# Optimization experiments

Hardware: AMD Instinct MI355X
Metric: run time of the kernel (lower is better)

The kernel has to match this reference:

```python
import jax, jax.numpy as jnp
import numpy as np

HEAD_NUM = 16
HIDDEN = 1024
HEAD_DIM = HIDDEN // HEAD_NUM


def setup_inputs() -> dict:
    key = jax.random.key(0)
    ks = jax.random.split(key, 9)
    B, S, D = 1, 4096, HIDDEN
    scale = 1.0 / np.sqrt(D)
    inp = {
        "x": jax.random.normal(ks[0], (B, S, D), jnp.float32),
        "wq": jax.random.normal(ks[1], (D, D), jnp.float32) * scale,
        "bq": jnp.zeros((D,), jnp.float32),
        "wk": jax.random.normal(ks[2], (D, D), jnp.float32) * scale,
        "bk": jnp.zeros((D,), jnp.float32),
        "wv": jax.random.normal(ks[3], (D, D), jnp.float32) * scale,
        "bv": jnp.zeros((D,), jnp.float32),
        "wo": jax.random.normal(ks[4], (D, D), jnp.float32) * scale,
        "bo": jnp.zeros((D,), jnp.float32),
    }
    return inp


def reference(x, wq, bq, wk, bk, wv, bv, wo, bo):
    B, S, D = x.shape
    H, Hd = HEAD_NUM, HEAD_DIM
    # QKV projections (weights stored as [in, out])
    q = (x @ wq + bq).reshape(B, S, H, Hd).transpose(0, 2, 1, 3)  # [B,H,S,Hd]
    k = (x @ wk + bk).reshape(B, S, H, Hd).transpose(0, 2, 1, 3)
    v = (x @ wv + bv).reshape(B, S, H, Hd).transpose(0, 2, 1, 3)
    scores = jnp.einsum("bhqd,bhkd->bhqk", q, k) / jnp.sqrt(jnp.float32(Hd))
    attn = jax.nn.softmax(scores, axis=-1)  # dropout in eval mode = identity
    out = jnp.einsum("bhqk,bhkd->bhqd", attn, v)
    out = out.transpose(0, 2, 1, 3).reshape(B, S, D)
    return out @ wo + bo
```

## Files before the change

### kernel.cpp

```cpp
#include <hip/hip_runtime.h>

#define S_LEN  4096
#define DMODEL 1024
#define NHEAD  16
#define HDIM   64

#define QSCALE 0.18033688011112042f

typedef unsigned short u16;
typedef unsigned int   u32;
typedef __bf16 bf16x8 __attribute__((ext_vector_type(8)));
typedef float  f32x4  __attribute__((ext_vector_type(4)));

static __device__ __forceinline__ u16 f2b(float f) {
    union { __bf16 b; u16 u; } c; c.b = (__bf16)f; return c.u;
}

static __device__ __forceinline__ float fexp2(float x) {
#if __has_builtin(__builtin_amdgcn_exp2f)
    return __builtin_amdgcn_exp2f(x);
#else
    return __expf(x * 0.6931471805599453f);
#endif
}

typedef __attribute__((address_space(3))) u32 lds_u32_t;
typedef __attribute__((address_space(1))) const u32 glb_u32_t;
static __device__ __forceinline__ void gload_lds16(const u16* g, u16* l) {
    __builtin_amdgcn_global_load_lds((glb_u32_t*)g, (lds_u32_t*)l, 16, 0, 0);
}

__global__ __launch_bounds__(256)
void convert_x(const float* __restrict__ x, u16* __restrict__ xb) {
    const int i0 = (blockIdx.x * 256 + threadIdx.x) * 8;
    float4 a = *reinterpret_cast<const float4*>(x + i0);
    float4 b = *reinterpret_cast<const float4*>(x + i0 + 4);
    u16 o[8] = {f2b(a.x), f2b(a.y), f2b(a.z), f2b(a.w),
                f2b(b.x), f2b(b.y), f2b(b.z), f2b(b.w)};
    *reinterpret_cast<uint4*>(xb + i0) = *reinterpret_cast<uint4*>(o);
}

__global__ __launch_bounds__(256)
void transpose_w4(const float* __restrict__ w0, const float* __restrict__ w1,
                  const float* __restrict__ w2, const float* __restrict__ w3,
                  u16* __restrict__ wT) {
    const int z = blockIdx.z;
    const float* w = (z == 0) ? w0 : (z == 1) ? w1 : (z == 2) ? w2 : w3;
    u16* dst0 = wT + (size_t)z * DMODEL * DMODEL;
    const int k0 = blockIdx.x * 64, n0 = blockIdx.y * 64;
    const int t = threadIdx.x;
    __shared__ u16 T[64][72];
    const int kk = t >> 4, nn = (t & 15) * 4;
    #pragma unroll
    for (int i = 0; i < 4; ++i) {
        float4 v = *reinterpret_cast<const float4*>(w + (size_t)(k0 + kk + i * 16) * DMODEL + n0 + nn);
        T[nn + 0][kk + i * 16] = f2b(v.x);
        T[nn + 1][kk + i * 16] = f2b(v.y);
        T[nn + 2][kk + i * 16] = f2b(v.z);
        T[nn + 3][kk + i * 16] = f2b(v.w);
    }
    __syncthreads();
    const int n = t >> 2, kc = (t & 3) * 16;
    uint4 r0 = *reinterpret_cast<const uint4*>(&T[n][kc]);
    uint4 r1 = *reinterpret_cast<const uint4*>(&T[n][kc + 8]);
    u16* dst = dst0 + (size_t)(n0 + n) * DMODEL + k0 + kc;
    *reinterpret_cast<uint4*>(dst)     = r0;
    *reinterpret_cast<uint4*>(dst + 8) = r1;
}

__global__ __launch_bounds__(256, 2)
void gemm_qkv(const u16* __restrict__ A, const u16* __restrict__ BT,
              const float* __restrict__ b0, const float* __restrict__ b1,
              const float* __restrict__ b2, u16* __restrict__ Cout) {
    const int m0 = blockIdx.x * 128;
    const int ny = blockIdx.y;
    const int tz = ny >> 3;
    const int n0 = (ny & 7) * 128;
    const int tid = threadIdx.x, lane = tid & 63, w = tid >> 6;
    const int wr = w >> 1, wc = w & 1;
    const int fm = lane & 15, fq = lane >> 4;

    __shared__ u16 As[128][32];
    __shared__ u16 Bs[128][32];

    const u16* Bb = BT + (size_t)tz * DMODEL * DMODEL;

    f32x4 acc[4][4];
    #pragma unroll
    for (int i = 0; i < 4; ++i)
        #pragma unroll
        for (int t = 0; t < 4; ++t) acc[i][t] = f32x4{0.f, 0.f, 0.f, 0.f};

    const int srow = lane >> 2, scol = (lane & 3) * 8;

    for (int k0 = 0; k0 < DMODEL; k0 += 32) {
        #pragma unroll
        for (int r = 0; r < 2; ++r) {
            const int rowA = w * 32 + r * 16;
            gload_lds16(A  + (size_t)(m0 + rowA + srow) * DMODEL + k0 + scol, &As[rowA][0]);
            gload_lds16(Bb + (size_t)(n0 + rowA + srow) * DMODEL + k0 + scol, &Bs[rowA][0]);
        }
        __syncthreads();
        bf16x8 af[4], bf[4];
        #pragma unroll
        for (int i = 0; i < 4; ++i) af[i] = *reinterpret_cast<const bf16x8*>(&As[wr * 64 + i * 16 + fm][fq * 8]);
        #pragma unroll
        for (int t = 0; t < 4; ++t) bf[t] = *reinterpret_cast<const bf16x8*>(&Bs[wc * 64 + t * 16 + fm][fq * 8]);
        #pragma unroll
        for (int i = 0; i < 4; ++i)
            #pragma unroll
            for (int t = 0; t < 4; ++t)
                acc[i][t] = __builtin_amdgcn_mfma_f32_16x16x32_bf16(af[i], bf[t], acc[i][t], 0, 0, 0);
        __syncthreads();
    }

    const float* bp = (tz == 0) ? b0 : (tz == 1) ? b1 : b2;
    u16* base = Cout + (size_t)tz * S_LEN * DMODEL;
    const float scl = (tz == 0) ? QSCALE : 1.0f;
    #pragma unroll
    for (int t = 0; t < 4; ++t) {
        const int col = n0 + wc * 64 + t * 16 + fm;
        const int hh = col >> 6, d = col & 63;
        const float bias = bp[col];
        if (tz == 2) {
            u16* vb = base + ((size_t)hh * HDIM + d) * S_LEN;
            #pragma unroll
            for (int i = 0; i < 4; ++i) {
                const int row0 = m0 + wr * 64 + i * 16 + fq * 4;
                u16 o[4] = {f2b(acc[i][t][0] + bias), f2b(acc[i][t][1] + bias),
                            f2b(acc[i][t][2] + bias), f2b(acc[i][t][3] + bias)};
                *reinterpret_cast<uint2*>(vb + row0) = *reinterpret_cast<uint2*>(o);
            }
        } else {
            #pragma unroll
            for (int i = 0; i < 4; ++i) {
                #pragma unroll
                for (int r = 0; r < 4; ++r) {
                    const int row = m0 + wr * 64 + i * 16 + fq * 4 + r;
                    base[((size_t)hh * S_LEN + row) * HDIM + d] =
                        f2b((acc[i][t][r] + bias) * scl);
                }
            }
        }
    }
}

__global__ __launch_bounds__(256, 2)
void gemm_o(const u16* __restrict__ A, const u16* __restrict__ BT,
            const float* __restrict__ bias, float* __restrict__ C) {
    const int m0 = blockIdx.x * 128;
    const int n0 = blockIdx.y * 64;
    const int tid = threadIdx.x, lane = tid & 63, w = tid >> 6;
    const int fm = lane & 15, fq = lane >> 4;

    __shared__ u16 As[128][32];
    __shared__ u16 Bs[64][32];

    f32x4 acc[2][4];
    #pragma unroll
    for (int i = 0; i < 2; ++i)
        #pragma unroll
        for (int t = 0; t < 4; ++t) acc[i][t] = f32x4{0.f, 0.f, 0.f, 0.f};

    const int srow = lane >> 2, scol = (lane & 3) * 8;

    for (int k0 = 0; k0 < DMODEL; k0 += 32) {
        #pragma unroll
        for (int r = 0; r < 2; ++r) {
            const int rowA = w * 32 + r * 16;
            gload_lds16(A + (size_t)(m0 + rowA + srow) * DMODEL + k0 + scol, &As[rowA][0]);
        }
        gload_lds16(BT + (size_t)(n0 + w * 16 + srow) * DMODEL + k0 + scol, &Bs[w * 16][0]);
        __syncthreads();
        bf16x8 af[2], bf[4];
        #pragma unroll
        for (int i = 0; i < 2; ++i) af[i] = *reinterpret_cast<const bf16x8*>(&As[w * 32 + i * 16 + fm][fq * 8]);
        #pragma unroll
        for (int t = 0; t < 4; ++t) bf[t] = *reinterpret_cast<const bf16x8*>(&Bs[t * 16 + fm][fq * 8]);
        #pragma unroll
        for (int i = 0; i < 2; ++i)
            #pragma unroll
            for (int t = 0; t < 4; ++t)
                acc[i][t] = __builtin_amdgcn_mfma_f32_16x16x32_bf16(af[i], bf[t], acc[i][t], 0, 0, 0);
        __syncthreads();
    }

    #pragma unroll
    for (int t = 0; t < 4; ++t) {
        const int col = n0 + t * 16 + fm;
        const float b = bias[col];
        #pragma unroll
        for (int i = 0; i < 2; ++i) {
            #pragma unroll
            for (int r = 0; r < 4; ++r) {
                const int row = m0 + w * 32 + i * 16 + fq * 4 + r;
                C[(size_t)row * DMODEL + col] = acc[i][t][r] + b;
            }
        }
    }
}

template<int NSPLIT>
__global__ __launch_bounds__(256, 4)
void attn_kernel(const u16* __restrict__ Q, const u16* __restrict__ K,
                 const u16* __restrict__ V, void* __restrict__ Optr,
                 float* __restrict__ Lp) {
    int qt, h, sp;
    if (NSPLIT > 1) {
        const int bid = blockIdx.x;
        const int xcd = bid & 7;
        const int g = bid >> 3;
        qt = g & 31;
        const int hs = g >> 5;
        h = xcd | ((hs & 1) << 3);
        sp = hs >> 1;
    } else {
        qt = blockIdx.x; h = blockIdx.y; sp = 0;
    }
    const int tid = threadIdx.x, lane = tid & 63, wid = tid >> 6;
    const int fm = lane & 15, fq = lane >> 4;

    __shared__ alignas(16) u16 Pt[128][36];
    __shared__ alignas(16) u16 Ks[64][68];
    __shared__ alignas(16) u16 Vt[64][68];

    const u16* Qh = Q + (size_t)h * S_LEN * HDIM;
    const u16* Kh = K + (size_t)h * S_LEN * HDIM;
    const u16* Vh = V + (size_t)h * S_LEN * HDIM;

    const int srow = tid >> 2, sch = (tid & 3) * 16;

    bf16x8 qf[2][2];
    #pragma unroll
    for (int rb = 0; rb < 2; ++rb) {
        const u16* qsrc = Qh + (size_t)(qt * 128 + wid * 32 + rb * 16 + fm) * HDIM + fq * 8;
        qf[rb][0] = *reinterpret_cast<const bf16x8*>(qsrc);
        qf[rb][1] = *reinterpret_cast<const bf16x8*>(qsrc + 32);
    }

    float rsum[2] = {0.f, 0.f};
    f32x4 oacc[2][4];
    #pragma unroll
    for (int rb = 0; rb < 2; ++rb)
        #pragma unroll
        for (int t = 0; t < 4; ++t) oacc[rb][t] = f32x4{0.f, 0.f, 0.f, 0.f};

    const int TOT  = S_LEN / 64;
    const int NT   = TOT / NSPLIT;
    const int kt0  = sp * NT;

    uint4 kr0, kr1, vr0, vr1;
    {
        const u16* ks = Kh + (size_t)(kt0 * 64 + srow) * HDIM + sch;
        kr0 = *reinterpret_cast<const uint4*>(ks);
        kr1 = *reinterpret_cast<const uint4*>(ks + 8);
        const u16* vs = Vh + (size_t)srow * S_LEN + kt0 * 64 + sch;
        vr0 = *reinterpret_cast<const uint4*>(vs);
        vr1 = *reinterpret_cast<const uint4*>(vs + 8);
    }

    for (int it = 0; it < NT; ++it) {
        const int kt = kt0 + it;
        __syncthreads();
        *reinterpret_cast<uint4*>(&Ks[srow][sch])     = kr0;
        *reinterpret_cast<uint4*>(&Ks[srow][sch + 8]) = kr1;
        *reinterpret_cast<uint4*>(&Vt[srow][sch])     = vr0;
        *reinterpret_cast<uint4*>(&Vt[srow][sch + 8]) = vr1;
        __syncthreads();

        if (it + 1 < NT) {
            const u16* ks = Kh + (size_t)((kt + 1) * 64 + srow) * HDIM + sch;
            kr0 = *reinterpret_cast<const uint4*>(ks);
            kr1 = *reinterpret_cast<const uint4*>(ks + 8);
            const u16* vs = Vh + (size_t)srow * S_LEN + (kt + 1) * 64 + sch;
            vr0 = *reinterpret_cast<const uint4*>(vs);
            vr1 = *reinterpret_cast<const uint4*>(vs + 8);
        }

        f32x4 sacc[2][4];
        #pragma unroll
        for (int rb = 0; rb < 2; ++rb)
            #pragma unroll
            for (int mt = 0; mt < 4; ++mt) sacc[rb][mt] = f32x4{0.f, 0.f, 0.f, 0.f};
        __builtin_amdgcn_s_setprio(1);
        #pragma unroll
        for (int kk2 = 0; kk2 < 2; ++kk2) {
            #pragma unroll
            for (int mt = 0; mt < 4; ++mt) {
                bf16x8 kf = *reinterpret_cast<const bf16x8*>(&Ks[mt * 16 + fm][kk2 * 32 + fq * 8]);
                #pragma unroll
                for (int rb = 0; rb < 2; ++rb)
                    sacc[rb][mt] = __builtin_amdgcn_mfma_f32_16x16x32_bf16(kf, qf[rb][kk2], sacc[rb][mt], 0, 0, 0);
            }
        }
        __builtin_amdgcn_s_setprio(0);

        #pragma unroll
        for (int ph = 0; ph < 2; ++ph) {
            #pragma unroll
            for (int rb = 0; rb < 2; ++rb) {
                #pragma unroll
                for (int m2 = 0; m2 < 2; ++m2) {
                    const int mt = ph * 2 + m2;
                    u32 pk[2];
                    float e0 = fexp2(sacc[rb][mt][0]);
                    float e1 = fexp2(sacc[rb][mt][1]);
                    float e2 = fexp2(sacc[rb][mt][2]);
                    float e3 = fexp2(sacc[rb][mt][3]);
                    rsum[rb] += (e0 + e1) + (e2 + e3);
                    pk[0] = (u32)f2b(e0) | ((u32)f2b(e1) << 16);
                    pk[1] = (u32)f2b(e2) | ((u32)f2b(e3) << 16);
                    *reinterpret_cast<uint2*>(&Pt[wid * 32 + rb * 16 + fm][m2 * 16 + fq * 4]) =
                        uint2{pk[0], pk[1]};
                }
            }
            bf16x8 af[2];
            #pragma unroll
            for (int rb = 0; rb < 2; ++rb)
                af[rb] = *reinterpret_cast<const bf16x8*>(&Pt[wid * 32 + rb * 16 + fm][fq * 8]);
            __builtin_amdgcn_s_setprio(1);
            #pragma unroll
            for (int t = 0; t < 4; ++t) {
                bf16x8 bf = *reinterpret_cast<const bf16x8*>(&Vt[t * 16 + fm][ph * 32 + fq * 8]);
                #pragma unroll
                for (int rb = 0; rb < 2; ++rb)
                    oacc[rb][t] = __builtin_amdgcn_mfma_f32_16x16x32_bf16(af[rb], bf, oacc[rb][t], 0, 0, 0);
            }
            __builtin_amdgcn_s_setprio(0);
        }
    }

    if (NSPLIT > 1) {
        float* Op = (float*)Optr + (size_t)sp * S_LEN * DMODEL;
        #pragma unroll
        for (int rb = 0; rb < 2; ++rb) {
            float rs = rsum[rb];
            rs += __shfl_xor(rs, 16, 64);
            rs += __shfl_xor(rs, 32, 64);
            if (fq == 0)
                Lp[(size_t)sp * NHEAD * S_LEN + (size_t)h * S_LEN +
                   qt * 128 + wid * 32 + rb * 16 + fm] = rs;
            #pragma unroll
            for (int t = 0; t < 4; ++t) {
                const int d = t * 16 + fm;
                #pragma unroll
                for (int r = 0; r < 4; ++r) {
                    const int row = qt * 128 + wid * 32 + rb * 16 + fq * 4 + r;
                    Op[(size_t)row * DMODEL + h * HDIM + d] = oacc[rb][t][r];
                }
            }
        }
    } else {
        float l[2][4];
        #pragma unroll
        for (int rb = 0; rb < 2; ++rb) {
            float rs = rsum[rb];
            rs += __shfl_xor(rs, 16, 64);
            rs += __shfl_xor(rs, 32, 64);
            #pragma unroll
            for (int r = 0; r < 4; ++r) l[rb][r] = __shfl(rs, fq * 4 + r, 64);
        }
        u16* O = (u16*)Optr;
        #pragma unroll
        for (int rb = 0; rb < 2; ++rb)
            #pragma unroll
            for (int t = 0; t < 4; ++t) {
                const int d = t * 16 + fm;
                #pragma unroll
                for (int r = 0; r < 4; ++r) {
                    const int row = qt * 128 + wid * 32 + rb * 16 + fq * 4 + r;
                    O[(size_t)row * DMODEL + h * HDIM + d] = f2b(oacc[rb][t][r] / l[rb][r]);
                }
            }
    }
}

template<int NS>
__global__ __launch_bounds__(256)
void combine_o(const float* __restrict__ Op, const float* __restrict__ Lp,
               u16* __restrict__ Ob) {
    const size_t i = ((size_t)blockIdx.x * 256 + threadIdx.x) * 4;
    const int row = (int)(i >> 10), col = (int)(i & 1023);
    const int h = col >> 6;
    float ax = 0.f, ay = 0.f, az = 0.f, aw = 0.f, l = 0.f;
    #pragma unroll
    for (int s = 0; s < NS; ++s) {
        float4 v = *reinterpret_cast<const float4*>(Op + (size_t)s * S_LEN * DMODEL + i);
        ax += v.x; ay += v.y; az += v.z; aw += v.w;
        l += Lp[(size_t)s * NHEAD * S_LEN + (size_t)h * S_LEN + row];
    }
    const float inv = 1.0f / l;
    u16 o[4] = {f2b(ax * inv), f2b(ay * inv), f2b(az * inv), f2b(aw * inv)};
    *reinterpret_cast<uint2*>(Ob + i) = *reinterpret_cast<uint2*>(o);
}

extern "C" void kernel_launch(void* const* d_in, const int* in_sizes, int n_in,
                              void* d_out, int out_size, void* d_ws, size_t ws_size,
                              hipStream_t stream) {
    const float* x  = (const float*)d_in[0];
    const float* wq = (const float*)d_in[1];
    const float* bq = (const float*)d_in[2];
    const float* wk = (const float*)d_in[3];
    const float* bk = (const float*)d_in[4];
    const float* wv = (const float*)d_in[5];
    const float* bv = (const float*)d_in[6];
    const float* wo = (const float*)d_in[7];
    const float* bo = (const float*)d_in[8];

    u16* ws = (u16*)d_ws;
    const size_t MW  = (size_t)DMODEL * DMODEL;
    const size_t NX  = (size_t)S_LEN * DMODEL;
    const size_t TSZ = (size_t)NHEAD * S_LEN * HDIM;

    u16* xb = ws;
    u16* WT = xb + NX;
    u16* Qb = WT + 4 * MW;
    u16* Ob = Qb + 3 * TSZ;
    float* Op = (float*)(Ob + NX);
    float* Lp2 = Op + (size_t)2 * NX;
    const size_t need2 = (size_t)((char*)(Lp2 + (size_t)2 * NHEAD * S_LEN) - (char*)d_ws);

    hipLaunchKernelGGL(convert_x, dim3(NX / 2048), dim3(256), 0, stream, x, xb);
    hipLaunchKernelGGL(transpose_w4, dim3(16, 16, 4), dim3(256), 0, stream, wq, wk, wv, wo, WT);

    hipLaunchKernelGGL(gemm_qkv, dim3(S_LEN / 128, 24), dim3(256), 0, stream,
                       xb, WT, bq, bk, bv, Qb);

    if (ws_size >= need2) {
        hipLaunchKernelGGL((attn_kernel<2>), dim3(1024), dim3(256), 0, stream,
                           Qb, Qb + TSZ, Qb + 2 * TSZ, (void*)Op, Lp2);
        hipLaunchKernelGGL((combine_o<2>), dim3((S_LEN * DMODEL / 4) / 256), dim3(256), 0, stream,
                           Op, Lp2, Ob);
    } else {
        hipLaunchKernelGGL((attn_kernel<1>), dim3(S_LEN / 128, NHEAD), dim3(256), 0, stream,
                           Qb, Qb + TSZ, Qb + 2 * TSZ, (void*)Ob, (float*)nullptr);
    }

    hipLaunchKernelGGL(gemm_o, dim3(S_LEN / 128, DMODEL / 64), dim3(256), 0, stream,
                       Ob, WT + 3 * MW, bo, (float*)d_out);
}
```

Measured before the change: 244.1 us.

## Load V fragments directly from global memory and double-buffer K tiles in LDS

Removes the V tile staging through shared memory. Each wave now loads its MFMA B-operand fragments for V straight from global (transposed V layout) into registers, issuing the second half after the QK MFMAs. K is double-buffered in LDS, which drops one of the two barriers per iteration. The cost is that every wave redundantly fetches the same V data from global/L2 instead of sharing one LDS copy, and register pressure rises.

Measured after the change: 347.7 us. +42.4%, slower.

```diff
diff --git a/kernel.cpp b/kernel.cpp
--- a/kernel.cpp
+++ b/kernel.cpp
@@ -221,8 +221,7 @@
     const int fm = lane & 15, fq = lane >> 4;
 
     __shared__ alignas(16) u16 Pt[128][36];
-    __shared__ alignas(16) u16 Ks[64][68];
-    __shared__ alignas(16) u16 Vt[64][68];
+    __shared__ alignas(16) u16 Ks[2][64][68];
 
     const u16* Qh = Q + (size_t)h * S_LEN * HDIM;
     const u16* Kh = K + (size_t)h * S_LEN * HDIM;
@@ -249,32 +248,34 @@
     const int NT   = TOT / NSPLIT;
     const int kt0  = sp * NT;
 
-    uint4 kr0, kr1, vr0, vr1;
+    const u16* vbase = Vh + (size_t)fm * S_LEN + (size_t)kt0 * 64 + fq * 8;
+
+    uint4 kr0, kr1;
     {
         const u16* ks = Kh + (size_t)(kt0 * 64 + srow) * HDIM + sch;
         kr0 = *reinterpret_cast<const uint4*>(ks);
         kr1 = *reinterpret_cast<const uint4*>(ks + 8);
-        const u16* vs = Vh + (size_t)srow * S_LEN + kt0 * 64 + sch;
-        vr0 = *reinterpret_cast<const uint4*>(vs);
-        vr1 = *reinterpret_cast<const uint4*>(vs + 8);
-    }
+    }
+
+    union vu { uint4 q; bf16x8 v; };
 
     for (int it = 0; it < NT; ++it) {
         const int kt = kt0 + it;
-        __syncthreads();
-        *reinterpret_cast<uint4*>(&Ks[srow][sch])     = kr0;
-        *reinterpret_cast<uint4*>(&Ks[srow][sch + 8]) = kr1;
-        *reinterpret_cast<uint4*>(&Vt[srow][sch])     = vr0;
-        *reinterpret_cast<uint4*>(&Vt[srow][sch + 8]) = vr1;
+        const int p = it & 1;
+
+        vu v0[4];
+        #pragma unroll
+        for (int t = 0; t < 4; ++t)
+            v0[t].q = *reinterpret_cast<const uint4*>(vbase + (size_t)(t * 16) * S_LEN);
+
+        *reinterpret_cast<uint4*>(&Ks[p][srow][sch])     = kr0;
+        *reinterpret_cast<uint4*>(&Ks[p][srow][sch + 8]) = kr1;
         __syncthreads();
 
         if (it + 1 < NT) {
             const u16* ks = Kh + (size_t)((kt + 1) * 64 + srow) * HDIM + sch;
             kr0 = *reinterpret_cast<const uint4*>(ks);
             kr1 = *reinterpret_cast<const uint4*>(ks + 8);
-            const u16* vs = Vh + (size_t)srow * S_LEN + (kt + 1) * 64 + sch;
-            vr0 = *reinterpret_cast<const uint4*>(vs);
-            vr1 = *reinterpret_cast<const uint4*>(vs + 8);
         }
 
         f32x4 sacc[2][4];
@@ -287,13 +288,18 @@
         for (int kk2 = 0; kk2 < 2; ++kk2) {
             #pragma unroll
             for (int mt = 0; mt < 4; ++mt) {
-                bf16x8 kf = *reinterpret_cast<const bf16x8*>(&Ks[mt * 16 + fm][kk2 * 32 + fq * 8]);
+                bf16x8 kf = *reinterpret_cast<const bf16x8*>(&Ks[p][mt * 16 + fm][kk2 * 32 + fq * 8]);
                 #pragma unroll
                 for (int rb = 0; rb < 2; ++rb)
                     sacc[rb][mt] = __builtin_amdgcn_mfma_f32_16x16x32_bf16(kf, qf[rb][kk2], sacc[rb][mt], 0, 0, 0);
             }
         }
         __builtin_amdgcn_s_setprio(0);
+
+        vu v1[4];
+        #pragma unroll
+        for (int t = 0; t < 4; ++t)
+            v1[t].q = *reinterpret_cast<const uint4*>(vbase + (size_t)(t * 16) * S_LEN + 32);
 
         #pragma unroll
         for (int ph = 0; ph < 2; ++ph) {
@@ -321,13 +327,15 @@
             __builtin_amdgcn_s_setprio(1);
             #pragma unroll
             for (int t = 0; t < 4; ++t) {
-                bf16x8 bf = *reinterpret_cast<const bf16x8*>(&Vt[t * 16 + fm][ph * 32 + fq * 8]);
+                bf16x8 bfv = (ph == 0) ? v0[t].v : v1[t].v;
                 #pragma unroll
                 for (int rb = 0; rb < 2; ++rb)
-                    oacc[rb][t] = __builtin_amdgcn_mfma_f32_16x16x32_bf16(af[rb], bf, oacc[rb][t], 0, 0, 0);
+                    oacc[rb][t] = __builtin_amdgcn_mfma_f32_16x16x32_bf16(af[rb], bfv, oacc[rb][t], 0, 0, 0);
             }
             __builtin_amdgcn_s_setprio(0);
         }
+
+        vbase += 64;
     }
 
     if (NSPLIT > 1) {
```
